# Kernel tuning notes

Measured on AMD Instinct MI355X. Metric: run time of the kernel, lower is better.

Reference implementation:

```python
import jax, jax.numpy as jnp
import numpy as np
from jax import lax

B, T, K, HID, NCLS = 32, 2048, 17, 64, 10
DILATIONS = (1, 1, 2)
RESIDUAL = (False, True, True)
TK = 3  # temporal kernel
BN_EPS = 1e-5
LN_EPS = 1e-5

COCO_EDGES = [(0,1),(0,2),(1,3),(2,4),(5,6),(5,7),(7,9),(6,8),(8,10),(5,11),(6,12),(11,13),(13,15),(12,14),(14,16)]

def build_skeleton_adj(num_kpts=K):
    adj = np.eye(num_kpts, dtype=np.float32)
    for i, j in COCO_EDGES:
        adj[i, j] = 1.0
        adj[j, i] = 1.0
    adj = adj + np.eye(num_kpts, dtype=np.float32)
    deg = adj.sum(axis=1, keepdims=True)
    deg[deg == 0] = 1.0
    return adj / deg

def setup_inputs() -> dict:
    key = jax.random.key(0)
    ks = jax.random.split(key, 8)
    kpts = jax.random.normal(ks[0], (B, T, K, 3), dtype=jnp.float32)
    adj = jnp.asarray(build_skeleton_adj(K))
    gcn_w0 = jax.random.normal(ks[1], (3, HID), dtype=jnp.float32) * (1.0 / np.sqrt(3))
    gcn_w1 = jax.random.normal(ks[2], (HID, HID), dtype=jnp.float32) * (1.0 / np.sqrt(HID))
    gcn_w2 = jax.random.normal(ks[3], (HID, HID), dtype=jnp.float32) * (1.0 / np.sqrt(HID))
    tcn_w = jax.random.normal(ks[4], (3, HID, HID, TK, 1), dtype=jnp.float32) * (1.0 / np.sqrt(HID * TK))
    bn_scale = 1.0 + 0.1 * jax.random.normal(ks[5], (3, HID), dtype=jnp.float32)
    bn_bias = 0.1 * jax.random.normal(ks[6], (3, HID), dtype=jnp.float32)
    bn_mean = 0.1 * jax.random.normal(ks[7], (3, HID), dtype=jnp.float32)
    bn_var = 0.5 + jax.random.uniform(jax.random.fold_in(key, 7), (3, HID), dtype=jnp.float32)
    ln_scale = jnp.ones((HID,), dtype=jnp.float32)
    ln_bias = jnp.zeros((HID,), dtype=jnp.float32)
    fc_w = jax.random.normal(jax.random.fold_in(key, 8), (HID, NCLS), dtype=jnp.float32) * (1.0 / np.sqrt(HID))
    fc_b = jnp.zeros((NCLS,), dtype=jnp.float32)
    return dict(kpts=kpts, adj=adj, gcn_w0=gcn_w0, gcn_w1=gcn_w1, gcn_w2=gcn_w2,
                tcn_w=tcn_w, bn_scale=bn_scale, bn_bias=bn_bias, bn_mean=bn_mean,
                bn_var=bn_var, ln_scale=ln_scale, ln_bias=ln_bias, fc_w=fc_w, fc_b=fc_b)

def _stgn_block(x, adj, gw, tw, bs, bb, bm, bv, dilation, residual):
    # x: [B, C_in, T, K]
    y = jnp.einsum('bctk,kv->bctv', x, adj)          # graph conv over keypoints
    y = jnp.einsum('bitk,io->botk', y, gw)           # channel mixing (intended GCN weight)
    pad = (TK - 1) * dilation // 2
    y = lax.conv_general_dilated(y, tw, window_strides=(1, 1),
                                 padding=[(pad, pad), (0, 0)],
                                 rhs_dilation=(dilation, 1),
                                 dimension_numbers=('NCHW', 'OIHW', 'NCHW'))
    inv = (bs / jnp.sqrt(bv + BN_EPS))[None, :, None, None]
    y = y * inv + (bb - bs * bm / jnp.sqrt(bv + BN_EPS))[None, :, None, None]
    y = jax.nn.relu(y)
    if residual:
        y = y + x
    return y

def reference(kpts, adj, gcn_w0, gcn_w1, gcn_w2, tcn_w, bn_scale, bn_bias, bn_mean,
              bn_var, ln_scale, ln_bias, fc_w, fc_b):
    x = jnp.transpose(kpts, (0, 3, 1, 2))  # [B, 3, T, K]
    gws = (gcn_w0, gcn_w1, gcn_w2)
    for i in range(3):
        x = _stgn_block(x, adj, gws[i], tcn_w[i], bn_scale[i], bn_bias[i],
                        bn_mean[i], bn_var[i], DILATIONS[i], RESIDUAL[i])
    feat = x.mean(axis=(2, 3))  # [B, HID] temporal/spatial mean pool
    mu = feat.mean(axis=-1, keepdims=True)
    var = feat.var(axis=-1, keepdims=True)
    feat = (feat - mu) / jnp.sqrt(var + LN_EPS) * ln_scale + ln_bias
    return feat @ fc_w + fc_b  # [B, NCLS]
```

## Files before the change

### kernel.cpp

```cpp
#include <hip/hip_runtime.h>
#include <hip/hip_fp16.h>
#include <math.h>

#define T_DIM 2048
#define TP_DIM 2052
#define K_DIM 17
#define HID   64
#define B_DIM 32

typedef short s16x8 __attribute__((ext_vector_type(8)));
typedef unsigned u32x2 __attribute__((ext_vector_type(2)));
typedef float f32x4 __attribute__((ext_vector_type(4)));
typedef _Float16 f16x2 __attribute__((ext_vector_type(2)));

__device__ __forceinline__ unsigned pkh(float lo, float hi) {
    return __builtin_bit_cast(unsigned, __builtin_amdgcn_cvt_pkrtz(lo, hi));
}
__device__ __forceinline__ f16x2 u2h(unsigned v) {
    return __builtin_bit_cast(f16x2, v);
}
__device__ __forceinline__ unsigned h2u(f16x2 v) {
    return __builtin_bit_cast(unsigned, v);
}
__device__ __forceinline__ short f2h(float f) {
    _Float16 h = (_Float16)f;
    return __builtin_bit_cast(short, h);
}

static constexpr int NBR_PTR[18] = {0,3,6,9,11,13,17,21,24,27,29,31,34,37,40,43,45,47};
static constexpr int NBR_K[47] = {
    0,1,2,  0,1,3,  0,2,4,  1,3,  2,4,
    5,6,7,11,  5,6,8,12,  5,7,9,  6,8,10,  7,9,  8,10,
    5,11,13,  6,12,14,  11,13,15,  12,14,16,  13,15,  14,16 };
__device__ const int d_NBR_PTR[18] = {0,3,6,9,11,13,17,21,24,27,29,31,34,37,40,43,45,47};
__device__ const int d_NBR_K[47] = {
    0,1,2,  0,1,3,  0,2,4,  1,3,  2,4,
    5,6,7,11,  5,6,8,12,  5,7,9,  6,8,10,  7,9,  8,10,
    5,11,13,  6,12,14,  11,13,15,  12,14,16,  13,15,  14,16 };

__global__ void fold_weights_kernel(
    const float* __restrict__ gw0, const float* __restrict__ gw1,
    const float* __restrict__ gw2, const float* __restrict__ tcn,
    const float* __restrict__ bns, const float* __restrict__ bnb,
    const float* __restrict__ bnm, const float* __restrict__ bnv,
    short* __restrict__ effT0, short* __restrict__ effT12,
    float* __restrict__ bnc)
{
    int tid = blockIdx.x * blockDim.x + threadIdx.x;
    int stride = gridDim.x * blockDim.x;
    for (int idx = tid; idx < 2048; idx += stride) {
        int o = idx >> 5, k = idx & 31, dt = k >> 3, cin = k & 7;
        float s = 0.f;
        if (dt < 3 && cin < 3)
            for (int m = 0; m < 64; m++)
                s += gw0[cin * 64 + m] * tcn[(o * 64 + m) * 3 + dt];
        effT0[idx] = f2h(s);
    }
    for (int idx = tid; idx < 24576; idx += stride) {
        int blk = idx / 12288;
        int r = idx - blk * 12288;
        int o = r / 192, k = r - o * 192, dt = k >> 6, c = k & 63;
        const float* gw = blk ? gw2 : gw1;
        const float* tw = tcn + (size_t)(blk + 1) * 64 * 64 * 3;
        float s = 0.f;
        for (int m = 0; m < 64; m++)
            s += gw[c * 64 + m] * tw[(o * 64 + m) * 3 + dt];
        effT12[idx] = f2h(s);
    }
    for (int i = tid; i < 192; i += stride) {
        float inv = bns[i] * rsqrtf(bnv[i] + 1e-5f);
        bnc[i] = inv;
        bnc[192 + i] = bnb[i] - bnm[i] * inv;
    }
}

__global__ __launch_bounds__(256) void premix_kernel(
    const float* __restrict__ x, const float* __restrict__ adj,
    float* __restrict__ xg, short* __restrict__ y2, int cb)
{
    const int idx = blockIdx.x * 256 + threadIdx.x;
    const int total = cb * TP_DIM * K_DIM;
    if (idx < total) {
        const int b = idx / (TP_DIM * K_DIM);
        const int rem = idx - b * (TP_DIM * K_DIM);
        const int tp = rem / K_DIM, j = rem - tp * K_DIM;
        const int t = tp - 2;
        float a0 = 0.f, a1 = 0.f, a2 = 0.f;
        if (t >= 0 && t < T_DIM) {
            const float* xp = x + ((size_t)b * T_DIM + t) * 51;
            const int p0 = d_NBR_PTR[j], p1 = d_NBR_PTR[j + 1];
            for (int e = p0; e < p1; e++) {
                int k = d_NBR_K[e];
                float w = adj[k * 17 + j];
                a0 += w * xp[k * 3 + 0];
                a1 += w * xp[k * 3 + 1];
                a2 += w * xp[k * 3 + 2];
            }
        }
        float* op = xg + ((size_t)b * TP_DIM + tp) * 52 + j * 3;
        op[0] = a0; op[1] = a1; op[2] = a2;
    }
    const int zn = cb * 4 * 1088;
    for (int z = idx; z < zn; z += gridDim.x * 256) {
        int bb = z / (4 * 1088);
        int rr = z - bb * 4 * 1088;
        int pi = rr / 1088;
        int ci = rr - pi * 1088;
        int tp = (pi < 2) ? pi : (2048 + pi);
        y2[((size_t)(bb * TP_DIM + tp) * K_DIM) * 64 + ci] = 0;
    }
}

__global__ __launch_bounds__(256, 4) void stgcn_ab_kernel(
    const float* __restrict__ xg, const float* __restrict__ adj,
    const short* __restrict__ effT0, const short* __restrict__ effT12,
    const float* __restrict__ bnc, short* __restrict__ y2)
{
    __shared__ unsigned adj_h[289];
    __shared__ __align__(16) float xtg[12 * 52];
    __shared__ __align__(16) short ybuf[170 * 72];

    const int tid = threadIdx.x;
    const int b = blockIdx.y;
    const int t0 = blockIdx.x * 8;
    const int lane = tid & 63, wave = tid >> 6;
    const int col = lane & 15, kgrp = lane >> 4;

    for (int i = tid; i < 289; i += 256) {
        float w = adj[i];
        adj_h[i] = pkh(w, w);
    }
    {
        const float4* src = (const float4*)(xg + ((size_t)b * TP_DIM + t0) * 52);
        float4* dst = (float4*)xtg;
        for (int i = tid; i < 156; i += 256) dst[i] = src[i];
    }
    s16x8 af1 = *(const s16x8*)(effT0 + (wave * 16 + col) * 32 + kgrp * 8);
    s16x8 af2[6];
    #pragma unroll
    for (int kk = 0; kk < 6; kk++)
        af2[kk] = *(const s16x8*)(effT12 +
            (wave * 16 + col) * 192 + kk * 32 + kgrp * 8);
    __syncthreads();

    {
        f32x4 inv4 = *(const f32x4*)&bnc[wave * 16 + kgrp * 4];
        f32x4 sh4  = *(const f32x4*)&bnc[192 + wave * 16 + kgrp * 4];
        for (int tile = 0; tile < 11; tile++) {
            const int r = tile * 16 + col;
            const int me = r < 170 ? r : 169;
            const int s = (me * 241) >> 12;
            const int j = me - s * 17;
            int4 bz = {0, 0, 0, 0};
            if (kgrp < 3) {
                const float* xp = &xtg[(s + kgrp) * 52 + j * 3];
                bz.x = (int)pkh(xp[0], xp[1]);
                bz.y = (int)pkh(xp[2], 0.f);
            }
            s16x8 bfr = __builtin_bit_cast(s16x8, bz);
            f32x4 acc = __builtin_amdgcn_mfma_f32_16x16x32_f16(
                af1, bfr, (f32x4){0.f, 0.f, 0.f, 0.f}, 0, 0, 0);
            const int t = t0 - 1 + s;
            const bool valid = (t >= 0) && (t < T_DIM);
            if (r < 170) {
                float v0 = valid ? fmaxf(acc[0] * inv4[0] + sh4[0], 0.f) : 0.f;
                float v1 = valid ? fmaxf(acc[1] * inv4[1] + sh4[1], 0.f) : 0.f;
                float v2 = valid ? fmaxf(acc[2] * inv4[2] + sh4[2], 0.f) : 0.f;
                float v3 = valid ? fmaxf(acc[3] * inv4[3] + sh4[3], 0.f) : 0.f;
                u32x2 st; st[0] = pkh(v0, v1); st[1] = pkh(v2, v3);
                *(u32x2*)&ybuf[r * 72 + wave * 16 + kgrp * 4] = st;
            }
        }
    }
    __syncthreads();

    f32x4 acc2[9];
    #pragma unroll
    for (int t2 = 0; t2 < 9; t2++) acc2[t2] = (f32x4){0.f, 0.f, 0.f, 0.f};
    #pragma unroll
    for (int kk = 0; kk < 6; kk++) {
        #pragma unroll
        for (int t2 = 0; t2 < 9; t2++) {
            const int r = t2 * 16 + col;
            const int me = r < 136 ? r : 135;
            s16x8 bfr = *(const s16x8*)&ybuf[
                (me + 17 * (kk >> 1)) * 72 + (kk & 1) * 32 + kgrp * 8];
            acc2[t2] = __builtin_amdgcn_mfma_f32_16x16x32_f16(
                af2[kk], bfr, acc2[t2], 0, 0, 0);
        }
    }
    unsigned rv[17];
    {
        const int tl = tid >> 5, o0 = (tid & 31) * 2;
        #pragma unroll
        for (int v = 0; v < 17; v++)
            rv[v] = *(const unsigned*)&ybuf[((tl + 1) * 17 + v) * 72 + o0];
    }
    __syncthreads();

    #pragma unroll
    for (int t2 = 0; t2 < 9; t2++) {
        const int r = t2 * 16 + col;
        if (r < 136) {
            u32x2 st;
            st[0] = pkh(acc2[t2][0], acc2[t2][1]);
            st[1] = pkh(acc2[t2][2], acc2[t2][3]);
            *(u32x2*)&ybuf[r * 72 + wave * 16 + kgrp * 4] = st;
        }
    }
    __syncthreads();

    {
        const int tl = tid >> 5, o0 = (tid & 31) * 2;
        const f16x2 inv2 = u2h(pkh(bnc[64 + o0], bnc[64 + o0 + 1]));
        const f16x2 sh2  = u2h(pkh(bnc[256 + o0], bnc[256 + o0 + 1]));
        const f16x2 zero = u2h(0u);
        f16x2 zk[17];
        #pragma unroll
        for (int k = 0; k < 17; k++)
            zk[k] = u2h(*(const unsigned*)&ybuf[(tl * 17 + k) * 72 + o0]);
        const size_t gout = ((size_t)b * TP_DIM + t0 + tl + 2) * K_DIM * 64;
        #pragma unroll
        for (int v = 0; v < 17; v++) {
            f16x2 g = zero;
            #pragma unroll
            for (int e = NBR_PTR[v]; e < NBR_PTR[v + 1]; e++) {
                int k = NBR_K[e];
                g = u2h(adj_h[k * 17 + v]) * zk[k] + g;
            }
            f16x2 val = __builtin_elementwise_max(g * inv2 + sh2, zero);
            val = val + u2h(rv[v]);
            *(unsigned*)&y2[gout + (size_t)v * 64 + o0] = h2u(val);
        }
    }
}

__global__ __launch_bounds__(256, 4) void stgcn_c_kernel(
    const short* __restrict__ y2, const float* __restrict__ adj,
    const short* __restrict__ effW3, const float* __restrict__ bnc,
    float* __restrict__ part, int b0)
{
    __shared__ unsigned adj_h[289];
    __shared__ __align__(16) short ybuf[204 * 72];

    float* pr = (float*)&ybuf[136 * 72];

    const int tid = threadIdx.x;
    const int b = blockIdx.y;
    const int t0 = blockIdx.x * 8;
    const int lane = tid & 63, wave = tid >> 6;
    const int col = lane & 15, kgrp = lane >> 4;

    for (int i = tid; i < 289; i += 256) {
        float w = adj[i];
        adj_h[i] = pkh(w, w);
    }
    s16x8 af3[6];
    #pragma unroll
    for (int kk = 0; kk < 6; kk++)
        af3[kk] = *(const s16x8*)(effW3 +
            (wave * 16 + col) * 192 + kk * 32 + kgrp * 8);

    {
        const short* base = y2 + ((size_t)b * TP_DIM + t0) * K_DIM * 64;
        for (int idx = tid; idx < 1632; idx += 256) {
            const int row = idx >> 3, c = idx & 7;
            *(s16x8*)&ybuf[row * 72 + c * 8] =
                *(const s16x8*)(base + (size_t)row * 64 + c * 8);
        }
    }
    __syncthreads();

    f32x4 acc3[9];
    #pragma unroll
    for (int t3 = 0; t3 < 9; t3++) acc3[t3] = (f32x4){0.f, 0.f, 0.f, 0.f};
    #pragma unroll
    for (int kk = 0; kk < 6; kk++) {
        #pragma unroll
        for (int t3 = 0; t3 < 9; t3++) {
            const int r = t3 * 16 + col;
            const int me = r < 136 ? r : 135;
            s16x8 bfr = *(const s16x8*)&ybuf[
                (me + 34 * (kk >> 1)) * 72 + (kk & 1) * 32 + kgrp * 8];
            acc3[t3] = __builtin_amdgcn_mfma_f32_16x16x32_f16(
                af3[kk], bfr, acc3[t3], 0, 0, 0);
        }
    }
    f16x2 rs = u2h(0u);
    {
        const int tl = tid >> 5, o0 = (tid & 31) * 2;
        #pragma unroll
        for (int v = 0; v < 17; v++)
            rs = rs + u2h(*(const unsigned*)&ybuf[((tl + 2) * 17 + v) * 72 + o0]);
    }
    __syncthreads();

    #pragma unroll
    for (int t3 = 0; t3 < 9; t3++) {
        const int r = t3 * 16 + col;
        if (r < 136) {
            u32x2 st;
            st[0] = pkh(acc3[t3][0], acc3[t3][1]);
            st[1] = pkh(acc3[t3][2], acc3[t3][3]);
            *(u32x2*)&ybuf[r * 72 + wave * 16 + kgrp * 4] = st;
        }
    }
    __syncthreads();

    {
        const int tl = tid >> 5, o0 = (tid & 31) * 2;
        const f16x2 inv2 = u2h(pkh(bnc[128 + o0], bnc[128 + o0 + 1]));
        const f16x2 sh2  = u2h(pkh(bnc[320 + o0], bnc[320 + o0 + 1]));
        const f16x2 zero = u2h(0u);
        f16x2 zk[17];
        #pragma unroll
        for (int k = 0; k < 17; k++)
            zk[k] = u2h(*(const unsigned*)&ybuf[(tl * 17 + k) * 72 + o0]);
        float ps0 = (float)rs[0], ps1 = (float)rs[1];
        #pragma unroll
        for (int v = 0; v < 17; v++) {
            f16x2 g = zero;
            #pragma unroll
            for (int e = NBR_PTR[v]; e < NBR_PTR[v + 1]; e++) {
                int k = NBR_K[e];
                g = u2h(adj_h[k * 17 + v]) * zk[k] + g;
            }
            f16x2 val = __builtin_elementwise_max(g * inv2 + sh2, zero);
            ps0 += (float)val[0];
            ps1 += (float)val[1];
        }
        *(float2*)&pr[tl * 64 + o0] = make_float2(ps0, ps1);
    }
    __syncthreads();
    if (tid < 64) {
        float s = 0.f;
        #pragma unroll
        for (int i = 0; i < 8; i++) s += pr[i * 64 + tid];
        part[((size_t)(b0 + b) * 256 + blockIdx.x) * 64 + tid] = s;
    }
}

__global__ __launch_bounds__(256) void finish_kernel(
    const float* __restrict__ part, const float* __restrict__ ln_s,
    const float* __restrict__ ln_b, const float* __restrict__ fc_w,
    const float* __restrict__ fc_b, float* __restrict__ out)
{
    __shared__ float red[4][64];
    __shared__ float ns[64];
    const int b = blockIdx.x;
    const int g = threadIdx.x >> 6, c = threadIdx.x & 63;
    float s = 0.f;
    for (int j = 0; j < 64; j++)
        s += part[((size_t)b * 256 + g * 64 + j) * 64 + c];
    red[g][c] = s;
    __syncthreads();
    if (threadIdx.x < 64) {
        float feat = (red[0][c] + red[1][c] + red[2][c] + red[3][c])
                   / (float)(T_DIM * K_DIM);
        float m = feat;
        #pragma unroll
        for (int off = 32; off > 0; off >>= 1) m += __shfl_down(m, off);
        m = __shfl(m, 0) / 64.f;
        float d = feat - m;
        float v = d * d;
        #pragma unroll
        for (int off = 32; off > 0; off >>= 1) v += __shfl_down(v, off);
        v = __shfl(v, 0) / 64.f;
        ns[c] = d * rsqrtf(v + 1e-5f) * ln_s[c] + ln_b[c];
    }
    __syncthreads();
    if (threadIdx.x < 10) {
        float o = fc_b[threadIdx.x];
        for (int i = 0; i < 64; i++) o += ns[i] * fc_w[i * 10 + threadIdx.x];
        out[b * 10 + threadIdx.x] = o;
    }
}

extern "C" void kernel_launch(void* const* d_in, const int* in_sizes, int n_in,
                              void* d_out, int out_size, void* d_ws, size_t ws_size,
                              hipStream_t stream)
{
    const float* kpts = (const float*)d_in[0];
    const float* adj  = (const float*)d_in[1];
    const float* gw0  = (const float*)d_in[2];
    const float* gw1  = (const float*)d_in[3];
    const float* gw2  = (const float*)d_in[4];
    const float* tcn  = (const float*)d_in[5];
    const float* bns  = (const float*)d_in[6];
    const float* bnb  = (const float*)d_in[7];
    const float* bnm  = (const float*)d_in[8];
    const float* bnv  = (const float*)d_in[9];
    const float* lns  = (const float*)d_in[10];
    const float* lnb  = (const float*)d_in[11];
    const float* fcw  = (const float*)d_in[12];
    const float* fcb  = (const float*)d_in[13];
    float* out = (float*)d_out;

    float* bnc  = (float*)d_ws;
    float* part = bnc + 384;
    short* effT0  = (short*)(part + (size_t)B_DIM * 256 * 64);
    short* effT12 = effT0 + 2048;
    float* xg     = (float*)(effT12 + 24576);
    const size_t fixed_bytes = 384 * 4 + (size_t)B_DIM * 256 * 64 * 4
                             + 2048 * 2 + 24576 * 2;
    const size_t xg_per_b = (size_t)TP_DIM * 52 * 4;
    const size_t y2_per_b = (size_t)TP_DIM * K_DIM * 64 * 2;

    int cb = B_DIM;
    while (cb > 1 &&
           fixed_bytes + (size_t)cb * (xg_per_b + y2_per_b) > ws_size)
        cb >>= 1;
    short* y2 = (short*)(xg + (size_t)cb * TP_DIM * 52);

    fold_weights_kernel<<<64, 256, 0, stream>>>(gw0, gw1, gw2, tcn,
                                                bns, bnb, bnm, bnv,
                                                effT0, effT12, bnc);

    const int pm_blocks = (cb * TP_DIM * K_DIM + 255) / 256;
    for (int b0 = 0; b0 < B_DIM; b0 += cb) {
        premix_kernel<<<pm_blocks, 256, 0, stream>>>(
            kpts + (size_t)b0 * T_DIM * K_DIM * 3, adj, xg, y2, cb);
        stgcn_ab_kernel<<<dim3(T_DIM / 8, cb), 256, 0, stream>>>(
            xg, adj, effT0, effT12, bnc, y2);
        stgcn_c_kernel<<<dim3(T_DIM / 8, cb), 256, 0, stream>>>(
            y2, adj, effT12 + 12288, bnc, part, b0);
    }

    finish_kernel<<<B_DIM, 256, 0, stream>>>(part, lns, lnb, fcw, fcb, out);
}
```

Baseline: 227.8 us.

## Fuse premix, blocks A/B and block C into one kernel with halo recompute

Merges the premix, first-two-block and third-block kernels into a single kernel per 8-timestep tile. Each tile loads raw keypoints with a wider temporal halo and recomputes the overlapping rows in shared memory, so the fp16 intermediate y2 and the xg buffer never go to global memory. This removes two launches and the global write and read of the large intermediate. In exchange it does redundant halo compute (238 and 204 rows instead of 170 and 136), uses more shared memory (occupancy bound lowered to 2), and drops the per-tile register accumulation in favour of sequential per-row loops.

```diff
diff --git a/kernel.cpp b/kernel.cpp
--- a/kernel.cpp
+++ b/kernel.cpp
@@ -3,7 +3,6 @@
 #include <math.h>
 
 #define T_DIM 2048
-#define TP_DIM 2052
 #define K_DIM 17
 #define HID   64
 #define B_DIM 32
@@ -74,51 +73,19 @@
     }
 }
 
-__global__ __launch_bounds__(256) void premix_kernel(
+__global__ __launch_bounds__(256, 2) void stgcn_fused_kernel(
     const float* __restrict__ x, const float* __restrict__ adj,
-    float* __restrict__ xg, short* __restrict__ y2, int cb)
-{
-    const int idx = blockIdx.x * 256 + threadIdx.x;
-    const int total = cb * TP_DIM * K_DIM;
-    if (idx < total) {
-        const int b = idx / (TP_DIM * K_DIM);
-        const int rem = idx - b * (TP_DIM * K_DIM);
-        const int tp = rem / K_DIM, j = rem - tp * K_DIM;
-        const int t = tp - 2;
-        float a0 = 0.f, a1 = 0.f, a2 = 0.f;
-        if (t >= 0 && t < T_DIM) {
-            const float* xp = x + ((size_t)b * T_DIM + t) * 51;
-            const int p0 = d_NBR_PTR[j], p1 = d_NBR_PTR[j + 1];
-            for (int e = p0; e < p1; e++) {
-                int k = d_NBR_K[e];
-                float w = adj[k * 17 + j];
-                a0 += w * xp[k * 3 + 0];
-                a1 += w * xp[k * 3 + 1];
-                a2 += w * xp[k * 3 + 2];
-            }
-        }
-        float* op = xg + ((size_t)b * TP_DIM + tp) * 52 + j * 3;
-        op[0] = a0; op[1] = a1; op[2] = a2;
-    }
-    const int zn = cb * 4 * 1088;
-    for (int z = idx; z < zn; z += gridDim.x * 256) {
-        int bb = z / (4 * 1088);
-        int rr = z - bb * 4 * 1088;
-        int pi = rr / 1088;
-        int ci = rr - pi * 1088;
-        int tp = (pi < 2) ? pi : (2048 + pi);
-        y2[((size_t)(bb * TP_DIM + tp) * K_DIM) * 64 + ci] = 0;
-    }
-}
-
-__global__ __launch_bounds__(256, 4) void stgcn_ab_kernel(
-    const float* __restrict__ xg, const float* __restrict__ adj,
     const short* __restrict__ effT0, const short* __restrict__ effT12,
-    const float* __restrict__ bnc, short* __restrict__ y2)
+    const short* __restrict__ effW3, const float* __restrict__ bnc,
+    float* __restrict__ part)
 {
     __shared__ unsigned adj_h[289];
-    __shared__ __align__(16) float xtg[12 * 52];
-    __shared__ __align__(16) short ybuf[170 * 72];
+    __shared__ float adj_f[289];
+    __shared__ __align__(16) float xs[16 * 51];
+    __shared__ __align__(16) float xtg[16 * 52];
+    __shared__ __align__(16) short y1buf[238 * 72];
+    __shared__ __align__(16) short y2buf[204 * 72];
+    float* const pr = xs;
 
     const int tid = threadIdx.x;
     const int b = blockIdx.y;
@@ -128,12 +95,16 @@
 
     for (int i = tid; i < 289; i += 256) {
         float w = adj[i];
+        adj_f[i] = w;
         adj_h[i] = pkh(w, w);
     }
     {
-        const float4* src = (const float4*)(xg + ((size_t)b * TP_DIM + t0) * 52);
-        float4* dst = (float4*)xtg;
-        for (int i = tid; i < 156; i += 256) dst[i] = src[i];
+        const float* src = x + ((size_t)b * T_DIM + t0 - 4) * 51;
+        for (int i = tid; i < 816; i += 256) {
+            const int row = i / 51;
+            const int t = t0 - 4 + row;
+            xs[i] = (t >= 0 && t < T_DIM) ? src[i] : 0.f;
+        }
     }
     s16x8 af1 = *(const s16x8*)(effT0 + (wave * 16 + col) * 32 + kgrp * 8);
     s16x8 af2[6];
@@ -143,12 +114,30 @@
             (wave * 16 + col) * 192 + kk * 32 + kgrp * 8);
     __syncthreads();
 
+    for (int i = tid; i < 272; i += 256) {
+        const int r = (i * 241) >> 12;
+        const int j = i - r * 17;
+        const float* xp = &xs[r * 51];
+        float a0 = 0.f, a1 = 0.f, a2 = 0.f;
+        const int p0 = d_NBR_PTR[j], p1 = d_NBR_PTR[j + 1];
+        for (int e = p0; e < p1; e++) {
+            const int k = d_NBR_K[e];
+            const float w = adj_f[k * 17 + j];
+            a0 += w * xp[k * 3 + 0];
+            a1 += w * xp[k * 3 + 1];
+            a2 += w * xp[k * 3 + 2];
+        }
+        float* op = &xtg[r * 52 + j * 3];
+        op[0] = a0; op[1] = a1; op[2] = a2;
+    }
+    __syncthreads();
+
     {
         f32x4 inv4 = *(const f32x4*)&bnc[wave * 16 + kgrp * 4];
         f32x4 sh4  = *(const f32x4*)&bnc[192 + wave * 16 + kgrp * 4];
-        for (int tile = 0; tile < 11; tile++) {
+        for (int tile = 0; tile < 15; tile++) {
             const int r = tile * 16 + col;
-            const int me = r < 170 ? r : 169;
+            const int me = r < 238 ? r : 237;
             const int s = (me * 241) >> 12;
             const int j = me - s * 17;
             int4 bz = {0, 0, 0, 0};
@@ -160,149 +149,97 @@
             s16x8 bfr = __builtin_bit_cast(s16x8, bz);
             f32x4 acc = __builtin_amdgcn_mfma_f32_16x16x32_f16(
                 af1, bfr, (f32x4){0.f, 0.f, 0.f, 0.f}, 0, 0, 0);
-            const int t = t0 - 1 + s;
+            const int t = t0 - 3 + s;
             const bool valid = (t >= 0) && (t < T_DIM);
-            if (r < 170) {
+            if (r < 238) {
                 float v0 = valid ? fmaxf(acc[0] * inv4[0] + sh4[0], 0.f) : 0.f;
                 float v1 = valid ? fmaxf(acc[1] * inv4[1] + sh4[1], 0.f) : 0.f;
                 float v2 = valid ? fmaxf(acc[2] * inv4[2] + sh4[2], 0.f) : 0.f;
                 float v3 = valid ? fmaxf(acc[3] * inv4[3] + sh4[3], 0.f) : 0.f;
                 u32x2 st; st[0] = pkh(v0, v1); st[1] = pkh(v2, v3);
-                *(u32x2*)&ybuf[r * 72 + wave * 16 + kgrp * 4] = st;
+                *(u32x2*)&y1buf[r * 72 + wave * 16 + kgrp * 4] = st;
             }
         }
     }
     __syncthreads();
 
-    f32x4 acc2[9];
-    #pragma unroll
-    for (int t2 = 0; t2 < 9; t2++) acc2[t2] = (f32x4){0.f, 0.f, 0.f, 0.f};
-    #pragma unroll
-    for (int kk = 0; kk < 6; kk++) {
-        #pragma unroll
-        for (int t2 = 0; t2 < 9; t2++) {
-            const int r = t2 * 16 + col;
-            const int me = r < 136 ? r : 135;
-            s16x8 bfr = *(const s16x8*)&ybuf[
+    for (int t2 = 0; t2 < 13; t2++) {
+        const int r = t2 * 16 + col;
+        const int me = r < 204 ? r : 203;
+        f32x4 acc = {0.f, 0.f, 0.f, 0.f};
+        #pragma unroll
+        for (int kk = 0; kk < 6; kk++) {
+            s16x8 bfr = *(const s16x8*)&y1buf[
                 (me + 17 * (kk >> 1)) * 72 + (kk & 1) * 32 + kgrp * 8];
-            acc2[t2] = __builtin_amdgcn_mfma_f32_16x16x32_f16(
-                af2[kk], bfr, acc2[t2], 0, 0, 0);
-        }
-    }
-    unsigned rv[17];
-    {
-        const int tl = tid >> 5, o0 = (tid & 31) * 2;
-        #pragma unroll
-        for (int v = 0; v < 17; v++)
-            rv[v] = *(const unsigned*)&ybuf[((tl + 1) * 17 + v) * 72 + o0];
-    }
-    __syncthreads();
-
-    #pragma unroll
-    for (int t2 = 0; t2 < 9; t2++) {
-        const int r = t2 * 16 + col;
-        if (r < 136) {
+            acc = __builtin_amdgcn_mfma_f32_16x16x32_f16(af2[kk], bfr, acc, 0, 0, 0);
+        }
+        if (r < 204) {
             u32x2 st;
-            st[0] = pkh(acc2[t2][0], acc2[t2][1]);
-            st[1] = pkh(acc2[t2][2], acc2[t2][3]);
-            *(u32x2*)&ybuf[r * 72 + wave * 16 + kgrp * 4] = st;
-        }
-    }
-    __syncthreads();
-
-    {
-        const int tl = tid >> 5, o0 = (tid & 31) * 2;
-        const f16x2 inv2 = u2h(pkh(bnc[64 + o0], bnc[64 + o0 + 1]));
-        const f16x2 sh2  = u2h(pkh(bnc[256 + o0], bnc[256 + o0 + 1]));
-        const f16x2 zero = u2h(0u);
-        f16x2 zk[17];
-        #pragma unroll
-        for (int k = 0; k < 17; k++)
-            zk[k] = u2h(*(const unsigned*)&ybuf[(tl * 17 + k) * 72 + o0]);
-        const size_t gout = ((size_t)b * TP_DIM + t0 + tl + 2) * K_DIM * 64;
-        #pragma unroll
-        for (int v = 0; v < 17; v++) {
-            f16x2 g = zero;
-            #pragma unroll
-            for (int e = NBR_PTR[v]; e < NBR_PTR[v + 1]; e++) {
-                int k = NBR_K[e];
-                g = u2h(adj_h[k * 17 + v]) * zk[k] + g;
-            }
-            f16x2 val = __builtin_elementwise_max(g * inv2 + sh2, zero);
-            val = val + u2h(rv[v]);
-            *(unsigned*)&y2[gout + (size_t)v * 64 + o0] = h2u(val);
-        }
-    }
-}
-
-__global__ __launch_bounds__(256, 4) void stgcn_c_kernel(
-    const short* __restrict__ y2, const float* __restrict__ adj,
-    const short* __restrict__ effW3, const float* __restrict__ bnc,
-    float* __restrict__ part, int b0)
-{
-    __shared__ unsigned adj_h[289];
-    __shared__ __align__(16) short ybuf[204 * 72];
-
-    float* pr = (float*)&ybuf[136 * 72];
-
-    const int tid = threadIdx.x;
-    const int b = blockIdx.y;
-    const int t0 = blockIdx.x * 8;
-    const int lane = tid & 63, wave = tid >> 6;
-    const int col = lane & 15, kgrp = lane >> 4;
-
-    for (int i = tid; i < 289; i += 256) {
-        float w = adj[i];
-        adj_h[i] = pkh(w, w);
+            st[0] = pkh(acc[0], acc[1]);
+            st[1] = pkh(acc[2], acc[3]);
+            *(u32x2*)&y2buf[r * 72 + wave * 16 + kgrp * 4] = st;
+        }
     }
     s16x8 af3[6];
     #pragma unroll
     for (int kk = 0; kk < 6; kk++)
         af3[kk] = *(const s16x8*)(effW3 +
             (wave * 16 + col) * 192 + kk * 32 + kgrp * 8);
-
-    {
-        const short* base = y2 + ((size_t)b * TP_DIM + t0) * K_DIM * 64;
-        for (int idx = tid; idx < 1632; idx += 256) {
-            const int row = idx >> 3, c = idx & 7;
-            *(s16x8*)&ybuf[row * 72 + c * 8] =
-                *(const s16x8*)(base + (size_t)row * 64 + c * 8);
-        }
-    }
-    __syncthreads();
-
-    f32x4 acc3[9];
-    #pragma unroll
-    for (int t3 = 0; t3 < 9; t3++) acc3[t3] = (f32x4){0.f, 0.f, 0.f, 0.f};
-    #pragma unroll
-    for (int kk = 0; kk < 6; kk++) {
-        #pragma unroll
-        for (int t3 = 0; t3 < 9; t3++) {
-            const int r = t3 * 16 + col;
-            const int me = r < 136 ? r : 135;
-            s16x8 bfr = *(const s16x8*)&ybuf[
-                (me + 34 * (kk >> 1)) * 72 + (kk & 1) * 32 + kgrp * 8];
-            acc3[t3] = __builtin_amdgcn_mfma_f32_16x16x32_f16(
-                af3[kk], bfr, acc3[t3], 0, 0, 0);
-        }
-    }
+    __syncthreads();
+
+    {
+        const f16x2 zero = u2h(0u);
+        for (int i = tid; i < 384; i += 256) {
+            const int tl = i >> 5, o0 = (i & 31) * 2;
+            const f16x2 inv2 = u2h(pkh(bnc[64 + o0], bnc[64 + o0 + 1]));
+            const f16x2 sh2  = u2h(pkh(bnc[256 + o0], bnc[256 + o0 + 1]));
+            f16x2 zk[17];
+            #pragma unroll
+            for (int k = 0; k < 17; k++)
+                zk[k] = u2h(*(const unsigned*)&y2buf[(tl * 17 + k) * 72 + o0]);
+            const int t = t0 - 2 + tl;
+            const bool valid = (t >= 0) && (t < T_DIM);
+            #pragma unroll
+            for (int v = 0; v < 17; v++) {
+                f16x2 g = zero;
+                #pragma unroll
+                for (int e = NBR_PTR[v]; e < NBR_PTR[v + 1]; e++) {
+                    int k = NBR_K[e];
+                    g = u2h(adj_h[k * 17 + v]) * zk[k] + g;
+                }
+                f16x2 val = __builtin_elementwise_max(g * inv2 + sh2, zero);
+                val = val + u2h(*(const unsigned*)&y1buf[
+                    ((tl + 1) * 17 + v) * 72 + o0]);
+                *(unsigned*)&y2buf[(tl * 17 + v) * 72 + o0] =
+                    valid ? h2u(val) : 0u;
+            }
+        }
+    }
+    __syncthreads();
+
     f16x2 rs = u2h(0u);
     {
         const int tl = tid >> 5, o0 = (tid & 31) * 2;
         #pragma unroll
         for (int v = 0; v < 17; v++)
-            rs = rs + u2h(*(const unsigned*)&ybuf[((tl + 2) * 17 + v) * 72 + o0]);
-    }
-    __syncthreads();
-
-    #pragma unroll
+            rs = rs + u2h(*(const unsigned*)&y2buf[((tl + 2) * 17 + v) * 72 + o0]);
+    }
+
     for (int t3 = 0; t3 < 9; t3++) {
         const int r = t3 * 16 + col;
+        const int me = r < 136 ? r : 135;
+        f32x4 acc = {0.f, 0.f, 0.f, 0.f};
+        #pragma unroll
+        for (int kk = 0; kk < 6; kk++) {
+            s16x8 bfr = *(const s16x8*)&y2buf[
+                (me + 34 * (kk >> 1)) * 72 + (kk & 1) * 32 + kgrp * 8];
+            acc = __builtin_amdgcn_mfma_f32_16x16x32_f16(af3[kk], bfr, acc, 0, 0, 0);
+        }
         if (r < 136) {
             u32x2 st;
-            st[0] = pkh(acc3[t3][0], acc3[t3][1]);
-            st[1] = pkh(acc3[t3][2], acc3[t3][3]);
-            *(u32x2*)&ybuf[r * 72 + wave * 16 + kgrp * 4] = st;
+            st[0] = pkh(acc[0], acc[1]);
+            st[1] = pkh(acc[2], acc[3]);
+            *(u32x2*)&y1buf[r * 72 + wave * 16 + kgrp * 4] = st;
         }
     }
     __syncthreads();
@@ -315,7 +252,7 @@
         f16x2 zk[17];
         #pragma unroll
         for (int k = 0; k < 17; k++)
-            zk[k] = u2h(*(const unsigned*)&ybuf[(tl * 17 + k) * 72 + o0]);
+            zk[k] = u2h(*(const unsigned*)&y1buf[(tl * 17 + k) * 72 + o0]);
         float ps0 = (float)rs[0], ps1 = (float)rs[1];
         #pragma unroll
         for (int v = 0; v < 17; v++) {
@@ -336,7 +273,7 @@
         float s = 0.f;
         #pragma unroll
         for (int i = 0; i < 8; i++) s += pr[i * 64 + tid];
-        part[((size_t)(b0 + b) * 256 + blockIdx.x) * 64 + tid] = s;
+        part[((size_t)b * 256 + blockIdx.x) * 64 + tid] = s;
     }
 }
 
@@ -400,31 +337,13 @@
     float* part = bnc + 384;
     short* effT0  = (short*)(part + (size_t)B_DIM * 256 * 64);
     short* effT12 = effT0 + 2048;
-    float* xg     = (float*)(effT12 + 24576);
-    const size_t fixed_bytes = 384 * 4 + (size_t)B_DIM * 256 * 64 * 4
-                             + 2048 * 2 + 24576 * 2;
-    const size_t xg_per_b = (size_t)TP_DIM * 52 * 4;
-    const size_t y2_per_b = (size_t)TP_DIM * K_DIM * 64 * 2;
-
-    int cb = B_DIM;
-    while (cb > 1 &&
-           fixed_bytes + (size_t)cb * (xg_per_b + y2_per_b) > ws_size)
-        cb >>= 1;
-    short* y2 = (short*)(xg + (size_t)cb * TP_DIM * 52);
 
     fold_weights_kernel<<<64, 256, 0, stream>>>(gw0, gw1, gw2, tcn,
                                                 bns, bnb, bnm, bnv,
                                                 effT0, effT12, bnc);
 
-    const int pm_blocks = (cb * TP_DIM * K_DIM + 255) / 256;
-    for (int b0 = 0; b0 < B_DIM; b0 += cb) {
-        premix_kernel<<<pm_blocks, 256, 0, stream>>>(
-            kpts + (size_t)b0 * T_DIM * K_DIM * 3, adj, xg, y2, cb);
-        stgcn_ab_kernel<<<dim3(T_DIM / 8, cb), 256, 0, stream>>>(
-            xg, adj, effT0, effT12, bnc, y2);
-        stgcn_c_kernel<<<dim3(T_DIM / 8, cb), 256, 0, stream>>>(
-            y2, adj, effT12 + 12288, bnc, part, b0);
-    }
+    stgcn_fused_kernel<<<dim3(T_DIM / 8, B_DIM), 256, 0, stream>>>(
+        kpts, adj, effT0, effT12, effT12 + 12288, bnc, part);
 
     finish_kernel<<<B_DIM, 256, 0, stream>>>(part, lns, lnb, fcw, fcb, out);
 }
```

After: 295.1 us. 29.5% more time.

## Fuse first-layer graph premix into stgcn_ab kernel and drop premix launch

Applied to the files above, without the earlier changes.

Removes the separate premix kernel that wrote adjacency-mixed input coordinates to a global xg buffer. Each stgcn_ab block now loads its raw keypoint rows (with zero padding at the time edges) into shared memory and computes the sparse graph mix locally. The y2 halo zeroing moves into the weight-fold kernel. This saves a launch and a global write and read round-trip. In exchange it adds extra shared memory and one more barrier per block, and the overlapping halo rows are recomputed by neighbouring blocks.

```diff
diff --git a/kernel.cpp b/kernel.cpp
--- a/kernel.cpp
+++ b/kernel.cpp
@@ -44,7 +44,7 @@
     const float* __restrict__ bns, const float* __restrict__ bnb,
     const float* __restrict__ bnm, const float* __restrict__ bnv,
     short* __restrict__ effT0, short* __restrict__ effT12,
-    float* __restrict__ bnc)
+    float* __restrict__ bnc, short* __restrict__ y2, int cb)
 {
     int tid = blockIdx.x * blockDim.x + threadIdx.x;
     int stride = gridDim.x * blockDim.x;
@@ -72,36 +72,8 @@
         bnc[i] = inv;
         bnc[192 + i] = bnb[i] - bnm[i] * inv;
     }
-}
-
-__global__ __launch_bounds__(256) void premix_kernel(
-    const float* __restrict__ x, const float* __restrict__ adj,
-    float* __restrict__ xg, short* __restrict__ y2, int cb)
-{
-    const int idx = blockIdx.x * 256 + threadIdx.x;
-    const int total = cb * TP_DIM * K_DIM;
-    if (idx < total) {
-        const int b = idx / (TP_DIM * K_DIM);
-        const int rem = idx - b * (TP_DIM * K_DIM);
-        const int tp = rem / K_DIM, j = rem - tp * K_DIM;
-        const int t = tp - 2;
-        float a0 = 0.f, a1 = 0.f, a2 = 0.f;
-        if (t >= 0 && t < T_DIM) {
-            const float* xp = x + ((size_t)b * T_DIM + t) * 51;
-            const int p0 = d_NBR_PTR[j], p1 = d_NBR_PTR[j + 1];
-            for (int e = p0; e < p1; e++) {
-                int k = d_NBR_K[e];
-                float w = adj[k * 17 + j];
-                a0 += w * xp[k * 3 + 0];
-                a1 += w * xp[k * 3 + 1];
-                a2 += w * xp[k * 3 + 2];
-            }
-        }
-        float* op = xg + ((size_t)b * TP_DIM + tp) * 52 + j * 3;
-        op[0] = a0; op[1] = a1; op[2] = a2;
-    }
     const int zn = cb * 4 * 1088;
-    for (int z = idx; z < zn; z += gridDim.x * 256) {
+    for (int z = tid; z < zn; z += stride) {
         int bb = z / (4 * 1088);
         int rr = z - bb * 4 * 1088;
         int pi = rr / 1088;
@@ -112,11 +84,13 @@
 }
 
 __global__ __launch_bounds__(256, 4) void stgcn_ab_kernel(
-    const float* __restrict__ xg, const float* __restrict__ adj,
+    const float* __restrict__ x, const float* __restrict__ adj,
     const short* __restrict__ effT0, const short* __restrict__ effT12,
     const float* __restrict__ bnc, short* __restrict__ y2)
 {
     __shared__ unsigned adj_h[289];
+    __shared__ float adj_f[289];
+    __shared__ __align__(16) float xs[12 * 51];
     __shared__ __align__(16) float xtg[12 * 52];
     __shared__ __align__(16) short ybuf[170 * 72];
 
@@ -128,12 +102,16 @@
 
     for (int i = tid; i < 289; i += 256) {
         float w = adj[i];
+        adj_f[i] = w;
         adj_h[i] = pkh(w, w);
     }
     {
-        const float4* src = (const float4*)(xg + ((size_t)b * TP_DIM + t0) * 52);
-        float4* dst = (float4*)xtg;
-        for (int i = tid; i < 156; i += 256) dst[i] = src[i];
+        const float* src = x + ((size_t)b * T_DIM + t0 - 2) * 51;
+        for (int i = tid; i < 612; i += 256) {
+            const int row = i / 51;
+            const int t = t0 - 2 + row;
+            xs[i] = (t >= 0 && t < T_DIM) ? src[i] : 0.f;
+        }
     }
     s16x8 af1 = *(const s16x8*)(effT0 + (wave * 16 + col) * 32 + kgrp * 8);
     s16x8 af2[6];
@@ -141,6 +119,24 @@
     for (int kk = 0; kk < 6; kk++)
         af2[kk] = *(const s16x8*)(effT12 +
             (wave * 16 + col) * 192 + kk * 32 + kgrp * 8);
+    __syncthreads();
+
+    for (int i = tid; i < 204; i += 256) {
+        const int r = (i * 241) >> 12;
+        const int j = i - r * 17;
+        const float* xp = &xs[r * 51];
+        float a0 = 0.f, a1 = 0.f, a2 = 0.f;
+        const int p0 = d_NBR_PTR[j], p1 = d_NBR_PTR[j + 1];
+        for (int e = p0; e < p1; e++) {
+            const int k = d_NBR_K[e];
+            const float w = adj_f[k * 17 + j];
+            a0 += w * xp[k * 3 + 0];
+            a1 += w * xp[k * 3 + 1];
+            a2 += w * xp[k * 3 + 2];
+        }
+        float* op = &xtg[r * 52 + j * 3];
+        op[0] = a0; op[1] = a1; op[2] = a2;
+    }
     __syncthreads();
 
     {
@@ -400,28 +396,22 @@
     float* part = bnc + 384;
     short* effT0  = (short*)(part + (size_t)B_DIM * 256 * 64);
     short* effT12 = effT0 + 2048;
-    float* xg     = (float*)(effT12 + 24576);
+    short* y2     = effT12 + 24576;
     const size_t fixed_bytes = 384 * 4 + (size_t)B_DIM * 256 * 64 * 4
                              + 2048 * 2 + 24576 * 2;
-    const size_t xg_per_b = (size_t)TP_DIM * 52 * 4;
     const size_t y2_per_b = (size_t)TP_DIM * K_DIM * 64 * 2;
 
     int cb = B_DIM;
-    while (cb > 1 &&
-           fixed_bytes + (size_t)cb * (xg_per_b + y2_per_b) > ws_size)
+    while (cb > 1 && fixed_bytes + (size_t)cb * y2_per_b > ws_size)
         cb >>= 1;
-    short* y2 = (short*)(xg + (size_t)cb * TP_DIM * 52);
 
     fold_weights_kernel<<<64, 256, 0, stream>>>(gw0, gw1, gw2, tcn,
                                                 bns, bnb, bnm, bnv,
-                                                effT0, effT12, bnc);
-
-    const int pm_blocks = (cb * TP_DIM * K_DIM + 255) / 256;
+                                                effT0, effT12, bnc, y2, cb);
+
     for (int b0 = 0; b0 < B_DIM; b0 += cb) {
-        premix_kernel<<<pm_blocks, 256, 0, stream>>>(
-            kpts + (size_t)b0 * T_DIM * K_DIM * 3, adj, xg, y2, cb);
         stgcn_ab_kernel<<<dim3(T_DIM / 8, cb), 256, 0, stream>>>(
-            xg, adj, effT0, effT12, bnc, y2);
+            kpts + (size_t)b0 * T_DIM * K_DIM * 3, adj, effT0, effT12, bnc, y2);
         stgcn_c_kernel<<<dim3(T_DIM / 8, cb), 256, 0, stream>>>(
             y2, adj, effT12 + 12288, bnc, part, b0);
     }
```

Result: no change. 230.6 us (+1.2%).
